# Kernel optimization log

Measured on AMD Instinct MI355X. Metric: run time of the kernel, lower is better.

Reference implementation:

```python
import jax, jax.numpy as jnp
import numpy as np

EPSILON = 1e-05


def setup_inputs() -> dict:
    key = jax.random.key(0)
    X = jax.random.normal(key, (4, 2048, 3), dtype=jnp.float32)
    K = jnp.ones((), dtype=jnp.float32)
    B = jnp.zeros((), dtype=jnp.float32)
    return {"X": X, "K": K, "B": B}


def reference(X, K, B):
    # X: [batch, N, D]
    delta_X = X[:, :, None, :] - X[:, None, :, :]          # [b, N, N, D]
    sq = jnp.sum(delta_X * delta_X, axis=-1, keepdims=True)  # [b, N, N, 1]
    # safe sqrt: distance is 0 on the diagonal; avoid nan-producing grad paths
    distance = jnp.sqrt(jnp.where(sq == 0, 1.0, sq))
    distance = jnp.where(sq == 0, 0.0, distance)
    direction = delta_X / (distance + EPSILON)
    force = (K * (distance - B)) * direction               # [b, N, N, D]
    aggregated_force = jnp.sum(force, axis=-2)             # [b, N, D]
    return X + aggregated_force
```

## Files before the change

### kernel.cpp

```cpp
#include <hip/hip_runtime.h>

#define NPTS 2048

__global__ __launch_bounds__(256) void spring_kernel(
    const float* __restrict__ X,
    const float* __restrict__ Kp,
    const float* __restrict__ Bp,
    float* __restrict__ out)
{
    __shared__ __align__(16) float xs[NPTS];
    __shared__ __align__(16) float ys[NPTS];
    __shared__ __align__(16) float zs[NPTS];

    const int tid    = threadIdx.x;
    const int b      = blockIdx.x >> 7;
    const int i_base = (blockIdx.x & 127) << 4;
    const float* Xb  = X + b * (NPTS * 3);

    for (int e = tid; e < NPTS * 3; e += 256) {
        float v = Xb[e];
        int n = e / 3;
        int c = e - n * 3;
        if (c == 0)      xs[n] = v;
        else if (c == 1) ys[n] = v;
        else             zs[n] = v;
    }
    __syncthreads();

    const float K  = Kp[0];
    const float KB = K * Bp[0];

    const int wv   = tid >> 6;
    const int lane = tid & 63;
    const int i0   = i_base + wv * 4;

    float xi[4], yi[4], zi[4];
    float ax[4] = {0.f,0.f,0.f,0.f};
    float ay[4] = {0.f,0.f,0.f,0.f};
    float az[4] = {0.f,0.f,0.f,0.f};
    #pragma unroll
    for (int q = 0; q < 4; ++q) {
        xi[q] = xs[i0 + q]; yi[q] = ys[i0 + q]; zi[q] = zs[i0 + q];
    }

    const float4* xs4 = (const float4*)xs;
    const float4* ys4 = (const float4*)ys;
    const float4* zs4 = (const float4*)zs;

    #pragma unroll 2
    for (int t = 0; t < NPTS / 4 / 64; ++t) {
        const int idx = t * 64 + lane;
        float4 jx = xs4[idx];
        float4 jy = ys4[idx];
        float4 jz = zs4[idx];
        const float jxa[4] = {jx.x, jx.y, jx.z, jx.w};
        const float jya[4] = {jy.x, jy.y, jy.z, jy.w};
        const float jza[4] = {jz.x, jz.y, jz.z, jz.w};

        #pragma unroll
        for (int c = 0; c < 4; ++c) {
            #pragma unroll
            for (int q = 0; q < 4; ++q) {
                float dx = xi[q] - jxa[c];
                float dy = yi[q] - jya[c];
                float dz = zi[q] - jza[c];
                float sq = fmaf(dx, dx, fmaf(dy, dy, dz * dz));
                sq = fmaxf(sq, 1e-30f);
                float r = __builtin_amdgcn_rsqf(sq);
                float s = fmaf(-KB, r, K);
                ax[q] = fmaf(dx, s, ax[q]);
                ay[q] = fmaf(dy, s, ay[q]);
                az[q] = fmaf(dz, s, az[q]);
            }
        }
    }

    #pragma unroll
    for (int q = 0; q < 4; ++q) {
        #pragma unroll
        for (int d = 32; d > 0; d >>= 1) {
            ax[q] += __shfl_down(ax[q], d, 64);
            ay[q] += __shfl_down(ay[q], d, 64);
            az[q] += __shfl_down(az[q], d, 64);
        }
    }

    if (lane == 0) {
        #pragma unroll
        for (int q = 0; q < 4; ++q) {
            float* o = out + (b * NPTS + i0 + q) * 3;
            o[0] = xi[q] + ax[q];
            o[1] = yi[q] + ay[q];
            o[2] = zi[q] + az[q];
        }
    }
}

extern "C" void kernel_launch(void* const* d_in, const int* in_sizes, int n_in,
                              void* d_out, int out_size, void* d_ws, size_t ws_size,
                              hipStream_t stream) {
    const float* X  = (const float*)d_in[0];
    const float* Kp = (const float*)d_in[1];
    const float* Bp = (const float*)d_in[2];
    float* out = (float*)d_out;

    dim3 grid(4 * (NPTS / 16));
    dim3 block(256);
    spring_kernel<<<grid, block, 0, stream>>>(X, Kp, Bp, out);
}
```

Baseline: 65.25 us.

## Halve rows per block, vectorize AoS-to-SoA staging, fold epsilon into FMA

Each block now handles 8 target points instead of 16, which doubles the grid to 1024 blocks, and each wave now does 2 rows instead of 4. The shared-memory staging loop reads float4 groups and transposes them into SoA with vector stores, replacing scalar loads that needed divide-by-3 indexing. The fmax clamp is folded into the FMA chain, and launch bounds now request 4 blocks per CU. In exchange, more blocks each reload the full point set into LDS, so staging traffic rises relative to compute.

```diff
diff --git a/kernel.cpp b/kernel.cpp
--- a/kernel.cpp
+++ b/kernel.cpp
@@ -2,7 +2,7 @@
 
 #define NPTS 2048
 
-__global__ __launch_bounds__(256) void spring_kernel(
+__global__ __launch_bounds__(256, 4) void spring_kernel(
     const float* __restrict__ X,
     const float* __restrict__ Kp,
     const float* __restrict__ Bp,
@@ -13,43 +13,48 @@
     __shared__ __align__(16) float zs[NPTS];
 
     const int tid    = threadIdx.x;
-    const int b      = blockIdx.x >> 7;
-    const int i_base = (blockIdx.x & 127) << 4;
+    const int b      = blockIdx.x >> 8;
+    const int i_base = (blockIdx.x & 255) << 3;
     const float* Xb  = X + b * (NPTS * 3);
-
-    for (int e = tid; e < NPTS * 3; e += 256) {
-        float v = Xb[e];
-        int n = e / 3;
-        int c = e - n * 3;
-        if (c == 0)      xs[n] = v;
-        else if (c == 1) ys[n] = v;
-        else             zs[n] = v;
-    }
-    __syncthreads();
 
     const float K  = Kp[0];
     const float KB = K * Bp[0];
 
+    {
+        const float4* Xb4 = (const float4*)Xb;
+        float4* xs4w = (float4*)xs;
+        float4* ys4w = (float4*)ys;
+        float4* zs4w = (float4*)zs;
+        #pragma unroll
+        for (int g0 = 0; g0 < NPTS / 4; g0 += 256) {
+            const int g = g0 + tid;
+            float4 f0 = Xb4[3 * g + 0];
+            float4 f1 = Xb4[3 * g + 1];
+            float4 f2 = Xb4[3 * g + 2];
+            xs4w[g] = make_float4(f0.x, f0.w, f1.z, f2.y);
+            ys4w[g] = make_float4(f0.y, f1.x, f1.w, f2.z);
+            zs4w[g] = make_float4(f0.z, f1.y, f2.x, f2.w);
+        }
+    }
+    __syncthreads();
+
     const int wv   = tid >> 6;
     const int lane = tid & 63;
-    const int i0   = i_base + wv * 4;
+    const int i0   = i_base + wv * 2;
 
-    float xi[4], yi[4], zi[4];
-    float ax[4] = {0.f,0.f,0.f,0.f};
-    float ay[4] = {0.f,0.f,0.f,0.f};
-    float az[4] = {0.f,0.f,0.f,0.f};
-    #pragma unroll
-    for (int q = 0; q < 4; ++q) {
-        xi[q] = xs[i0 + q]; yi[q] = ys[i0 + q]; zi[q] = zs[i0 + q];
-    }
+    const float xi0 = xs[i0],     yi0 = ys[i0],     zi0 = zs[i0];
+    const float xi1 = xs[i0 + 1], yi1 = ys[i0 + 1], zi1 = zs[i0 + 1];
+
+    float ax0 = 0.f, ay0 = 0.f, az0 = 0.f;
+    float ax1 = 0.f, ay1 = 0.f, az1 = 0.f;
 
     const float4* xs4 = (const float4*)xs;
     const float4* ys4 = (const float4*)ys;
     const float4* zs4 = (const float4*)zs;
 
-    #pragma unroll 2
+    #pragma unroll 4
     for (int t = 0; t < NPTS / 4 / 64; ++t) {
-        const int idx = t * 64 + lane;
+        const int idx = (t << 6) + lane;
         float4 jx = xs4[idx];
         float4 jy = ys4[idx];
         float4 jz = zs4[idx];
@@ -59,40 +64,49 @@
 
         #pragma unroll
         for (int c = 0; c < 4; ++c) {
-            #pragma unroll
-            for (int q = 0; q < 4; ++q) {
-                float dx = xi[q] - jxa[c];
-                float dy = yi[q] - jya[c];
-                float dz = zi[q] - jza[c];
-                float sq = fmaf(dx, dx, fmaf(dy, dy, dz * dz));
-                sq = fmaxf(sq, 1e-30f);
-                float r = __builtin_amdgcn_rsqf(sq);
-                float s = fmaf(-KB, r, K);
-                ax[q] = fmaf(dx, s, ax[q]);
-                ay[q] = fmaf(dy, s, ay[q]);
-                az[q] = fmaf(dz, s, az[q]);
+            {
+                float dx = xi0 - jxa[c];
+                float dy = yi0 - jya[c];
+                float dz = zi0 - jza[c];
+                float sq = fmaf(dx, dx, fmaf(dy, dy, fmaf(dz, dz, 1e-30f)));
+                float r  = __builtin_amdgcn_rsqf(sq);
+                float s  = fmaf(-KB, r, K);
+                ax0 = fmaf(dx, s, ax0);
+                ay0 = fmaf(dy, s, ay0);
+                az0 = fmaf(dz, s, az0);
+            }
+            {
+                float dx = xi1 - jxa[c];
+                float dy = yi1 - jya[c];
+                float dz = zi1 - jza[c];
+                float sq = fmaf(dx, dx, fmaf(dy, dy, fmaf(dz, dz, 1e-30f)));
+                float r  = __builtin_amdgcn_rsqf(sq);
+                float s  = fmaf(-KB, r, K);
+                ax1 = fmaf(dx, s, ax1);
+                ay1 = fmaf(dy, s, ay1);
+                az1 = fmaf(dz, s, az1);
             }
         }
     }
 
     #pragma unroll
-    for (int q = 0; q < 4; ++q) {
-        #pragma unroll
-        for (int d = 32; d > 0; d >>= 1) {
-            ax[q] += __shfl_down(ax[q], d, 64);
-            ay[q] += __shfl_down(ay[q], d, 64);
-            az[q] += __shfl_down(az[q], d, 64);
-        }
+    for (int d = 32; d > 0; d >>= 1) {
+        ax0 += __shfl_down(ax0, d, 64);
+        ay0 += __shfl_down(ay0, d, 64);
+        az0 += __shfl_down(az0, d, 64);
+        ax1 += __shfl_down(ax1, d, 64);
+        ay1 += __shfl_down(ay1, d, 64);
+        az1 += __shfl_down(az1, d, 64);
     }
 
     if (lane == 0) {
-        #pragma unroll
-        for (int q = 0; q < 4; ++q) {
-            float* o = out + (b * NPTS + i0 + q) * 3;
-            o[0] = xi[q] + ax[q];
-            o[1] = yi[q] + ay[q];
-            o[2] = zi[q] + az[q];
-        }
+        float* o = out + (b * NPTS + i0) * 3;
+        o[0] = xi0 + ax0;
+        o[1] = yi0 + ay0;
+        o[2] = zi0 + az0;
+        o[3] = xi1 + ax1;
+        o[4] = yi1 + ay1;
+        o[5] = zi1 + az1;
     }
 }
 
@@ -104,7 +118,7 @@
     const float* Bp = (const float*)d_in[2];
     float* out = (float*)d_out;
 
-    dim3 grid(4 * (NPTS / 16));
+    dim3 grid(4 * (NPTS / 8));
     dim3 block(256);
     spring_kernel<<<grid, block, 0, stream>>>(X, Kp, Bp, out);
 }
```

New measurement: 63.27 us. 3.0% less time.
